# Kernel tuning notes

Hardware: AMD Instinct MI355X
Metric: run time of the kernel (lower is better)

Reference implementation:

```python
import jax, jax.numpy as jnp
import numpy as np

KS_LIST = (7, 9, 11)
DILS = (1, 2, 4, 8, 16, 32)
PER = 5          # kernels per (kernel_size, dilation) group
EPS = 1e-5       # BatchNorm1d eps
N, C, L = 512, 12, 8192


def _rocket_features(x, W7, b7, W9, b9, W11, b11):
    # x: [N, C, L]; W_ks: [6*PER, C, ks]; b_ks: [6*PER]
    dn = ('NCH', 'OIH', 'NCH')
    feats = []
    for W, b in ((W7, b7), (W9, b9), (W11, b11)):
        for j, d in enumerate(DILS):
            w = W[j * PER:(j + 1) * PER]      # [PER, C, ks]
            bb = b[j * PER:(j + 1) * PER]     # [PER]
            # one dilated conv for all PER kernels in this group -> [N, PER, L]
            out = jax.lax.conv_general_dilated(
                x, w, window_strides=(1,), padding='SAME',
                rhs_dilation=(d,), dimension_numbers=dn) + bb[None, :, None]
            ppv = jnp.mean((out > 0).astype(x.dtype), axis=2)  # [N, PER]
            mx = jnp.max(out, axis=2)                          # [N, PER]
            # interleave (ppv_k, max_k) per kernel, matching the torch loop order
            feats.append(jnp.stack([ppv, mx], axis=-1).reshape(x.shape[0], 2 * PER))
    f = jnp.concatenate(feats, axis=1)  # [N, 2*nb_kernels] = [N, 180]
    # BatchNorm1d(affine=False), training mode: batch stats, biased variance
    mean = jnp.mean(f, axis=0)
    var = jnp.var(f, axis=0)
    return (f - mean) / jnp.sqrt(var + EPS)


def setup_inputs() -> dict:
    key = jax.random.key(0)
    kx, k1, k2, k3, k4, k5, k6 = jax.random.split(key, 7)
    G = len(DILS) * PER  # 30 kernels per kernel-size family
    inp = {
        'x': jax.random.normal(kx, (N, C, L), dtype=jnp.float32),
        'W7': jax.random.uniform(k1, (G, C, 7), minval=-1.0, maxval=1.0, dtype=jnp.float32),
        'b7': jax.random.normal(k2, (G,), dtype=jnp.float32),
        'W9': jax.random.uniform(k3, (G, C, 9), minval=-1.0, maxval=1.0, dtype=jnp.float32),
        'b9': jax.random.normal(k4, (G,), dtype=jnp.float32),
        'W11': jax.random.uniform(k5, (G, C, 11), minval=-1.0, maxval=1.0, dtype=jnp.float32),
        'b11': jax.random.normal(k6, (G,), dtype=jnp.float32),
    }
    return inp


def reference(x, W7, b7, W9, b9, W11, b11):
    return _rocket_features(x, W7, b7, W9, b9, W11, b11)
```

## Files before the change

### kernel.cpp

```cpp
#include <hip/hip_runtime.h>
#include <math.h>
#include <limits.h>

#define N_SAMP 512
#define C_IN   12
#define L_IN   8192
#define NDIL   6
#define NFILT  30
#define NFEAT  180
#define NCHUNK 4
#define CHUNK  (L_IN / NCHUNK)
#define EPSV   1e-5f

#define HALO   160
#define TLC    256
#define LWC    (TLC + 2*HALO)
#define TILEB  (LWC * 16)

#define WF_OFF (3 * N_SAMP * NCHUNK * NFILT * 2)
#define WTAB_B (NDIL * 3 * 64 * 16)

typedef __attribute__((ext_vector_type(4))) int i32x4;

__device__ __forceinline__ int swz(int r) {
    return (r << 4) ^ ((((r >> 3) ^ (r >> 6)) & 7) << 4);
}

__global__ __launch_bounds__(256)
void build_wb(const float* __restrict__ W7, const float* __restrict__ W9,
              const float* __restrict__ W11, const float* __restrict__ b7,
              const float* __restrict__ b9, const float* __restrict__ b11,
              signed char* __restrict__ wc, signed char* __restrict__ wd,
              float* __restrict__ bias_tab)
{
    const int t = blockIdx.x * 256 + threadIdx.x;
    if (t < NDIL * 3 * 64) {
        const int j    = t / 192;
        const int mf   = (t / 64) % 3;
        const int lane = t % 64;
        const int col  = lane & 15;
        const int q    = lane >> 4;
        const int tap  = mf * 4 + q;
#pragma unroll
        for (int e = 0; e < 16; ++e) {
            float v = 0.0f;
            if (col < 15 && tap <= 10 && e < 12) {
                const int toff = tap - 5;
                if (col < 5) {
                    if (toff >= -3 && toff <= 3)
                        v = W7[((j * 5 + col) * 12 + e) * 7 + toff + 3];
                } else if (col < 10) {
                    if (toff >= -4 && toff <= 4)
                        v = W9[((j * 5 + col - 5) * 12 + e) * 9 + toff + 4];
                } else {
                    v = W11[((j * 5 + col - 10) * 12 + e) * 11 + toff + 5];
                }
            }
            const int W  = __float2int_rn(v * 8192.0f);
            const int C8 = (W + 128) >> 8;
            const int D8 = W - (C8 << 8);
            wc[(size_t)t * 16 + e] = (signed char)C8;
            wd[(size_t)t * 16 + e] = (signed char)D8;
        }
    } else if (t < NDIL * 3 * 64 + 96) {
        const int i = t - NDIL * 3 * 64;
        const int j = i / 16, s = i % 16;
        float b = 0.0f;
        if (s < 5)       b = b7 [j * 5 + s];
        else if (s < 10) b = b9 [j * 5 + s - 5];
        else if (s < 15) b = b11[j * 5 + s - 10];
        bias_tab[j * 16 + s] = b;
    }
}

__global__ __launch_bounds__(256)
void rocket_conv_i8(const float* __restrict__ x,
                    const signed char* __restrict__ wc,
                    const signed char* __restrict__ wd,
                    const float* __restrict__ bias_tab,
                    float* __restrict__ ws)
{
    __shared__ __align__(16) signed char xq[2][TILEB];
    __shared__ int scnt[NDIL * 16];
    __shared__ int smx [NDIL * 16];

    const int ch  = blockIdx.x;
    const int n   = blockIdx.y;
    const int tid = threadIdx.x;
    const int lane = tid & 63, wv = tid >> 6;
    const int row_l = lane & 15, q = lane >> 4;
    const float* __restrict__ xrow = x + (size_t)n * C_IN * L_IN;
    const i32x4* __restrict__ wcv = (const i32x4*)wc;
    const i32x4* __restrict__ wdv = (const i32x4*)wd;

    if (tid < NDIL * 16) {
        scnt[tid] = 0;
        smx[tid]  = INT_MIN;
    }

    const int c0 = ch * CHUNK;
#pragma unroll 1
    for (int st = 0; st < CHUNK / TLC; ++st) {
        const int t0 = c0 + st * TLC;
        __syncthreads();
#pragma unroll 1
        for (int r = tid; r < LWC; r += 256) {
            const int g = t0 - HALO + r;
            int h[4] = {0, 0, 0, 0}, l[4] = {0, 0, 0, 0};
            if ((unsigned)g < (unsigned)L_IN) {
#pragma unroll
                for (int c = 0; c < 12; ++c) {
                    const float xv = xrow[c * L_IN + g];
                    const int X  = __float2int_rn(xv * 4096.0f);
                    const int A8 = (X + 128) >> 8;
                    const int B8 = X - (A8 << 8);
                    h[c >> 2] |= (A8 & 255) << ((c & 3) * 8);
                    l[c >> 2] |= (B8 & 255) << ((c & 3) * 8);
                }
            }
            const int cell = swz(r);
            *(i32x4*)&xq[0][cell] = (i32x4){h[0], h[1], h[2], h[3]};
            *(i32x4*)&xq[1][cell] = (i32x4){l[0], l[1], l[2], l[3]};
        }
        __syncthreads();

#pragma unroll 1
        for (int j = 0; j < NDIL; ++j) {
            const int d = 1 << j;
            const i32x4 C0 = wcv[(j * 3 + 0) * 64 + lane];
            const i32x4 C1 = wcv[(j * 3 + 1) * 64 + lane];
            const i32x4 C2 = wcv[(j * 3 + 2) * 64 + lane];
            const i32x4 D0 = wdv[(j * 3 + 0) * 64 + lane];
            const i32x4 D1 = wdv[(j * 3 + 1) * 64 + lane];
            const i32x4 D2 = wdv[(j * 3 + 2) * 64 + lane];
            const float bj = bias_tab[j * 16 + row_l];
            const int tj = (int)floorf(bj * -33554432.0f);
            const int r0 = HALO + wv * 64 + row_l + (q - 5) * d;
            const int r1 = HALO + wv * 64 + row_l + (q - 1) * d;
            const int r2 = HALO + wv * 64 + row_l +
                           ((q == 3) ? 0 : (q + 3) * d);

            int cnt_i = 0, mx_i = INT_MIN;
#pragma unroll
            for (int t = 0; t < 4; ++t) {
                const int cell0 = swz(r0 + 16 * t);
                const int cell1 = swz(r1 + 16 * t);
                const int cell2 = swz(r2 + 16 * t);
                i32x4 a0 = {0, 0, 0, 0};
                i32x4 a1 = {0, 0, 0, 0};
                i32x4 a2 = {0, 0, 0, 0};
                {
                    i32x4 ah = *(const i32x4*)&xq[0][cell0];
                    i32x4 al = *(const i32x4*)&xq[1][cell0];
                    a0 = __builtin_amdgcn_mfma_i32_16x16x64_i8(ah, C0, a0, 0, 0, 0);
                    a1 = __builtin_amdgcn_mfma_i32_16x16x64_i8(ah, D0, a1, 0, 0, 0);
                    a1 = __builtin_amdgcn_mfma_i32_16x16x64_i8(al, C0, a1, 0, 0, 0);
                    a2 = __builtin_amdgcn_mfma_i32_16x16x64_i8(al, D0, a2, 0, 0, 0);
                }
                {
                    i32x4 ah = *(const i32x4*)&xq[0][cell1];
                    i32x4 al = *(const i32x4*)&xq[1][cell1];
                    a0 = __builtin_amdgcn_mfma_i32_16x16x64_i8(ah, C1, a0, 0, 0, 0);
                    a1 = __builtin_amdgcn_mfma_i32_16x16x64_i8(ah, D1, a1, 0, 0, 0);
                    a1 = __builtin_amdgcn_mfma_i32_16x16x64_i8(al, C1, a1, 0, 0, 0);
                    a2 = __builtin_amdgcn_mfma_i32_16x16x64_i8(al, D1, a2, 0, 0, 0);
                }
                {
                    i32x4 ah = *(const i32x4*)&xq[0][cell2];
                    i32x4 al = *(const i32x4*)&xq[1][cell2];
                    a0 = __builtin_amdgcn_mfma_i32_16x16x64_i8(ah, C2, a0, 0, 0, 0);
                    a1 = __builtin_amdgcn_mfma_i32_16x16x64_i8(ah, D2, a1, 0, 0, 0);
                    a1 = __builtin_amdgcn_mfma_i32_16x16x64_i8(al, C2, a1, 0, 0, 0);
                    a2 = __builtin_amdgcn_mfma_i32_16x16x64_i8(al, D2, a2, 0, 0, 0);
                }
                int t01, t23;
                {
                    const int v0 = (a0[0] << 16) + (a1[0] << 8) + a2[0];
                    const int v1 = (a0[1] << 16) + (a1[1] << 8) + a2[1];
                    const int v2 = (a0[2] << 16) + (a1[2] << 8) + a2[2];
                    const int v3 = (a0[3] << 16) + (a1[3] << 8) + a2[3];
                    cnt_i += (v0 > tj) + (v1 > tj) + (v2 > tj) + (v3 > tj);
                    t01 = (v0 > v1) ? v0 : v1;
                    t23 = (v2 > v3) ? v2 : v3;
                }
                const int tmx = (t01 > t23) ? t01 : t23;
                mx_i = (tmx > mx_i) ? tmx : mx_i;
            }

            cnt_i += __shfl_xor(cnt_i, 16);
            cnt_i += __shfl_xor(cnt_i, 32);
            {
                int o = __shfl_xor(mx_i, 16);  mx_i = (o > mx_i) ? o : mx_i;
                o     = __shfl_xor(mx_i, 32);  mx_i = (o > mx_i) ? o : mx_i;
            }
            if (lane < 16) {
                atomicAdd(&scnt[j * 16 + lane], cnt_i);
                atomicMax(&smx[j * 16 + lane], mx_i);
            }
        }
    }

    __syncthreads();
    if (tid < 96) {
        const int jj = tid >> 4, s = tid & 15;
        if (s < 15) {
            const int c = scnt[jj * 16 + s];
            const int m = smx[jj * 16 + s];
            const float bj = bias_tab[jj * 16 + s];
            const int ks = s / 5, f = s % 5;
            const int gg = jj * 5 + f;
            const size_t base =
                ((((size_t)ks * N_SAMP + n) * NCHUNK + ch) * NFILT + gg) * 2;
            ws[base]     = (float)c;
            ws[base + 1] = bj + (float)m * 2.9802322387695312e-8f;
        }
    }
}

__global__ __launch_bounds__(512)
void rocket_finish(const float* __restrict__ ws, float* __restrict__ out)
{
    const int i = blockIdx.x;
    const int t = threadIdx.x;

    const int ks = i / 60;
    const int r  = i % 60;
    const int g  = r >> 1;
    const int m  = r & 1;

    const size_t base =
        ((((size_t)ks * N_SAMP + t) * NCHUNK) * NFILT + g) * 2 + m;

    float v;
    if (m) {
        v = -INFINITY;
#pragma unroll
        for (int c = 0; c < NCHUNK; ++c)
            v = fmaxf(v, ws[base + (size_t)c * NFILT * 2]);
    } else {
        v = 0.0f;
#pragma unroll
        for (int c = 0; c < NCHUNK; ++c)
            v += ws[base + (size_t)c * NFILT * 2];
        v *= (1.0f / (float)L_IN);
    }

    float s  = v;
    float sq = v * v;
#pragma unroll
    for (int off = 32; off; off >>= 1) {
        s  += __shfl_xor(s, off);
        sq += __shfl_xor(sq, off);
    }

    __shared__ float ss[8], sqq[8];
    const int lane = t & 63;
    const int wv   = t >> 6;
    if (lane == 0) { ss[wv] = s; sqq[wv] = sq; }
    __syncthreads();
    if (t == 0) {
        float S = 0.0f, Q = 0.0f;
#pragma unroll
        for (int w = 0; w < 8; ++w) { S += ss[w]; Q += sqq[w]; }
        ss[0] = S; sqq[0] = Q;
    }
    __syncthreads();

    const float mean = ss[0] * (1.0f / (float)N_SAMP);
    const float var  = sqq[0] * (1.0f / (float)N_SAMP) - mean * mean;
    out[t * NFEAT + i] = (v - mean) / sqrtf(var + EPSV);
}

extern "C" void kernel_launch(void* const* d_in, const int* in_sizes, int n_in,
                              void* d_out, int out_size, void* d_ws, size_t ws_size,
                              hipStream_t stream)
{
    const float* x   = (const float*)d_in[0];
    const float* W7  = (const float*)d_in[1];
    const float* b7  = (const float*)d_in[2];
    const float* W9  = (const float*)d_in[3];
    const float* b9  = (const float*)d_in[4];
    const float* W11 = (const float*)d_in[5];
    const float* b11 = (const float*)d_in[6];
    float* out = (float*)d_out;
    float* ws  = (float*)d_ws;
    signed char* wc = (signed char*)(ws + WF_OFF);
    signed char* wd = wc + WTAB_B;
    float* bias_tab = (float*)(wd + WTAB_B);

    build_wb<<<5, 256, 0, stream>>>(W7, W9, W11, b7, b9, b11, wc, wd, bias_tab);

    dim3 grid(NCHUNK, N_SAMP);
    rocket_conv_i8<<<grid, 256, 0, stream>>>(x, wc, wd, bias_tab, ws);

    rocket_finish<<<NFEAT, 512, 0, stream>>>(ws, out);
}
```

Measured before the change: 300.8 us.

## Double-buffer LDS tiles and prefetch next tile's inputs into registers during MFMA compute

Doubles the shared-memory tile buffer and issues the global loads for the next tile into registers before the current tile's dilation loop, quantizing and writing them to the other buffer afterward. One barrier per tile is removed. The aim is to hide global-load latency behind MFMA work. The cost is 36 extra float registers per thread and twice the LDS, which may reduce occupancy.

```diff
diff --git a/kernel.cpp b/kernel.cpp
--- a/kernel.cpp
+++ b/kernel.cpp
@@ -16,6 +16,7 @@
 #define TLC    256
 #define LWC    (TLC + 2*HALO)
 #define TILEB  (LWC * 16)
+#define NST    (CHUNK / TLC)
 
 #define WF_OFF (3 * N_SAMP * NCHUNK * NFILT * 2)
 #define WTAB_B (NDIL * 3 * 64 * 16)
@@ -80,7 +81,7 @@
                     const float* __restrict__ bias_tab,
                     float* __restrict__ ws)
 {
-    __shared__ __align__(16) signed char xq[2][TILEB];
+    __shared__ __align__(16) signed char xq[2][2][TILEB];
     __shared__ int scnt[NDIL * 16];
     __shared__ int smx [NDIL * 16];
 
@@ -93,36 +94,64 @@
     const i32x4* __restrict__ wcv = (const i32x4*)wc;
     const i32x4* __restrict__ wdv = (const i32x4*)wd;
 
-    if (tid < NDIL * 16) {
-        scnt[tid] = 0;
-        smx[tid]  = INT_MIN;
-    }
+    if (tid < NDIL * 16) { scnt[tid] = 0; smx[tid] = INT_MIN; }
 
     const int c0 = ch * CHUNK;
+
+    float xv0[12], xv1[12], xv2[12];
+
+#define LOADS(ST)                                                         \
+    {                                                                     \
+        const int gb = c0 + (ST) * TLC - HALO + tid;                      \
+        _Pragma("unroll")                                                 \
+        for (int c = 0; c < 12; ++c)                                      \
+            xv0[c] = ((unsigned)gb < (unsigned)L_IN)                      \
+                         ? xrow[c * L_IN + gb] : 0.0f;                    \
+        _Pragma("unroll")                                                 \
+        for (int c = 0; c < 12; ++c)                                      \
+            xv1[c] = ((unsigned)(gb + 256) < (unsigned)L_IN)              \
+                         ? xrow[c * L_IN + gb + 256] : 0.0f;              \
+        if (tid < LWC - 512) {                                            \
+            _Pragma("unroll")                                             \
+            for (int c = 0; c < 12; ++c)                                  \
+                xv2[c] = ((unsigned)(gb + 512) < (unsigned)L_IN)          \
+                             ? xrow[c * L_IN + gb + 512] : 0.0f;          \
+        }                                                                 \
+    }
+
+#define QWRITE_ROW(BUF, XV, ROFF)                                        \
+    {                                                                    \
+        int h[4] = {0, 0, 0, 0}, l[4] = {0, 0, 0, 0};                    \
+        _Pragma("unroll")                                                \
+        for (int c = 0; c < 12; ++c) {                                   \
+            const int X  = __float2int_rn((XV)[c] * 4096.0f);            \
+            const int A8 = (X + 128) >> 8;                \
+            const int B8 = X - (A8 << 8);               \
+            h[c >> 2] |= (A8 & 255) << ((c & 3) * 8);                    \
+            l[c >> 2] |= (B8 & 255) << ((c & 3) * 8);                    \
+        }                                                                \
+        const int cell_ = swz(tid + (ROFF));                             \
+        *(i32x4*)&xq[(BUF)][0][cell_] = (i32x4){h[0], h[1], h[2], h[3]}; \
+        *(i32x4*)&xq[(BUF)][1][cell_] = (i32x4){l[0], l[1], l[2], l[3]}; \
+    }
+
+#define QWRITE(BUF)                                                      \
+    {                                                                    \
+        QWRITE_ROW(BUF, xv0, 0)                                          \
+        QWRITE_ROW(BUF, xv1, 256)                                        \
+        if (tid < LWC - 512) QWRITE_ROW(BUF, xv2, 512)                   \
+    }
+
+    LOADS(0);
+    QWRITE(0);
+    __syncthreads();
+
 #pragma unroll 1
-    for (int st = 0; st < CHUNK / TLC; ++st) {
-        const int t0 = c0 + st * TLC;
-        __syncthreads();
-#pragma unroll 1
-        for (int r = tid; r < LWC; r += 256) {
-            const int g = t0 - HALO + r;
-            int h[4] = {0, 0, 0, 0}, l[4] = {0, 0, 0, 0};
-            if ((unsigned)g < (unsigned)L_IN) {
-#pragma unroll
-                for (int c = 0; c < 12; ++c) {
-                    const float xv = xrow[c * L_IN + g];
-                    const int X  = __float2int_rn(xv * 4096.0f);
-                    const int A8 = (X + 128) >> 8;
-                    const int B8 = X - (A8 << 8);
-                    h[c >> 2] |= (A8 & 255) << ((c & 3) * 8);
-                    l[c >> 2] |= (B8 & 255) << ((c & 3) * 8);
-                }
-            }
-            const int cell = swz(r);
-            *(i32x4*)&xq[0][cell] = (i32x4){h[0], h[1], h[2], h[3]};
-            *(i32x4*)&xq[1][cell] = (i32x4){l[0], l[1], l[2], l[3]};
-        }
-        __syncthreads();
+    for (int st = 0; st < NST; ++st) {
+        if (st + 1 < NST) LOADS(st + 1);
+
+        const signed char* __restrict__ xa = &xq[st & 1][0][0];
+        const signed char* __restrict__ xb = &xq[st & 1][1][0];
 
 #pragma unroll 1
         for (int j = 0; j < NDIL; ++j) {
@@ -150,24 +179,24 @@
                 i32x4 a1 = {0, 0, 0, 0};
                 i32x4 a2 = {0, 0, 0, 0};
                 {
-                    i32x4 ah = *(const i32x4*)&xq[0][cell0];
-                    i32x4 al = *(const i32x4*)&xq[1][cell0];
+                    i32x4 ah = *(const i32x4*)&xa[cell0];
+                    i32x4 al = *(const i32x4*)&xb[cell0];
                     a0 = __builtin_amdgcn_mfma_i32_16x16x64_i8(ah, C0, a0, 0, 0, 0);
                     a1 = __builtin_amdgcn_mfma_i32_16x16x64_i8(ah, D0, a1, 0, 0, 0);
                     a1 = __builtin_amdgcn_mfma_i32_16x16x64_i8(al, C0, a1, 0, 0, 0);
                     a2 = __builtin_amdgcn_mfma_i32_16x16x64_i8(al, D0, a2, 0, 0, 0);
                 }
                 {
-                    i32x4 ah = *(const i32x4*)&xq[0][cell1];
-                    i32x4 al = *(const i32x4*)&xq[1][cell1];
+                    i32x4 ah = *(const i32x4*)&xa[cell1];
+                    i32x4 al = *(const i32x4*)&xb[cell1];
                     a0 = __builtin_amdgcn_mfma_i32_16x16x64_i8(ah, C1, a0, 0, 0, 0);
                     a1 = __builtin_amdgcn_mfma_i32_16x16x64_i8(ah, D1, a1, 0, 0, 0);
                     a1 = __builtin_amdgcn_mfma_i32_16x16x64_i8(al, C1, a1, 0, 0, 0);
                     a2 = __builtin_amdgcn_mfma_i32_16x16x64_i8(al, D1, a2, 0, 0, 0);
                 }
                 {
-                    i32x4 ah = *(const i32x4*)&xq[0][cell2];
-                    i32x4 al = *(const i32x4*)&xq[1][cell2];
+                    i32x4 ah = *(const i32x4*)&xa[cell2];
+                    i32x4 al = *(const i32x4*)&xb[cell2];
                     a0 = __builtin_amdgcn_mfma_i32_16x16x64_i8(ah, C2, a0, 0, 0, 0);
                     a1 = __builtin_amdgcn_mfma_i32_16x16x64_i8(ah, D2, a1, 0, 0, 0);
                     a1 = __builtin_amdgcn_mfma_i32_16x16x64_i8(al, C2, a1, 0, 0, 0);
@@ -198,9 +227,11 @@
                 atomicMax(&smx[j * 16 + lane], mx_i);
             }
         }
-    }
-
-    __syncthreads();
+
+        if (st + 1 < NST) QWRITE((st + 1) & 1);
+        __syncthreads();
+    }
+
     if (tid < 96) {
         const int jj = tid >> 4, s = tid & 15;
         if (s < 15) {
@@ -215,6 +246,9 @@
             ws[base + 1] = bj + (float)m * 2.9802322387695312e-8f;
         }
     }
+#undef LOADS
+#undef QWRITE_ROW
+#undef QWRITE
 }
 
 __global__ __launch_bounds__(512)
```

Result: slower. 309.6 us (+2.9%).
